# Kernel optimization log

Measured on AMD Instinct MI355X. Metric: run time of the kernel, lower is better.

Reference implementation:

```python
import jax, jax.numpy as jnp
import numpy as np

DIM = 1024
NUM_HEADS = 16
HEAD_DIM = DIM // NUM_HEADS
SCALE = HEAD_DIM ** -0.5


def setup_inputs() -> dict:
    key = jax.random.key(0)
    ks = jax.random.split(key, 5)
    x = jax.random.normal(ks[0], (4, 1024, DIM), dtype=jnp.float32)
    w_qkv = jax.random.normal(ks[1], (DIM, 3 * DIM), dtype=jnp.float32) * (DIM ** -0.5)
    b_qkv = jnp.zeros((3 * DIM,), dtype=jnp.float32)
    w_proj = jax.random.normal(ks[2], (DIM, DIM), dtype=jnp.float32) * (DIM ** -0.5)
    b_proj = jnp.zeros((DIM,), dtype=jnp.float32)
    return {"x": x, "w_qkv": w_qkv, "b_qkv": b_qkv, "w_proj": w_proj, "b_proj": b_proj}


def reference(x, w_qkv, b_qkv, w_proj, b_proj):
    B, N, C = x.shape
    qkv = x @ w_qkv + b_qkv                                  # [B, N, 3C]
    qkv = qkv.reshape(B, N, 3, NUM_HEADS, HEAD_DIM)
    qkv = jnp.transpose(qkv, (2, 0, 3, 1, 4))                # [3, B, H, N, d]
    q, k, v = qkv[0] * SCALE, qkv[1], qkv[2]
    # attn scores in float32 (clamp to finfo range is a no-op after the cast)
    attn = jnp.einsum('bhnd,bhmd->bhnm', q, k).astype(jnp.float32)
    f32 = jnp.finfo(jnp.float32)
    attn = jnp.clip(attn, f32.min, f32.max)
    attn = jax.nn.softmax(attn, axis=-1)
    out = jnp.einsum('bhnm,bhmd->bhnd', attn, v)             # [B, H, N, d]
    out = jnp.transpose(out, (0, 2, 1, 3)).reshape(B, N, C)
    return out @ w_proj + b_proj
```

## Files before the change

kernel.cpp:

```cpp
#include <hip/hip_runtime.h>


typedef _Float16 half8 __attribute__((ext_vector_type(8)));
typedef _Float16 half4v __attribute__((ext_vector_type(4)));
typedef __fp16 fp16x2 __attribute__((ext_vector_type(2)));
typedef float floatx4 __attribute__((ext_vector_type(4)));

#define MFMA16(a, b, c) __builtin_amdgcn_mfma_f32_16x16x32_f16((a), (b), (c), 0, 0, 0)

static constexpr int DIM = 1024;
static constexpr int BATCH = 4;
static constexpr int SEQ = 1024;
static constexpr int NH = 16;
static constexpr int HD = 64;
static constexpr float SCALE = 0.125f;

__device__ static inline void gld16(_Float16* lds, const _Float16* g) {
    __builtin_amdgcn_global_load_lds(
        (const __attribute__((address_space(1))) void*)g,
        (__attribute__((address_space(3))) void*)lds, 16, 0, 0);
}

__global__ __launch_bounds__(256) void prep(const float* __restrict__ x,
                                            _Float16* __restrict__ xh,
                                            const float* __restrict__ wqkv,
                                            _Float16* __restrict__ wqkvT,
                                            const float* __restrict__ wproj,
                                            _Float16* __restrict__ wprojT) {
    __shared__ float tile[32][33];
    const int bid = blockIdx.x;
    const int tid = threadIdx.x;
    if (bid < 4096) {
        int i = (bid * 256 + tid) * 4;
        float4 v = *reinterpret_cast<const float4*>(x + i);
        half4v h;
        h[0] = (_Float16)v.x; h[1] = (_Float16)v.y;
        h[2] = (_Float16)v.z; h[3] = (_Float16)v.w;
        const int m = i >> 10, k = i & 1023;
        *reinterpret_cast<half4v*>(
            &xh[((size_t)(k >> 5) * 4096 + m) * 32 + (k & 31)]) = h;
        return;
    }
    const float* in;
    _Float16* out;
    int C, NN, bx, by;
    if (bid < 7168) {
        int b = bid - 4096;
        in = wqkv; out = wqkvT; C = 3072; NN = 3072;
        bx = b % 96; by = b / 96;
    } else {
        int b = bid - 7168;
        in = wproj; out = wprojT; C = 1024; NN = 1024;
        bx = b & 31; by = b >> 5;
    }
    const int c0 = bx * 32, r0 = by * 32;
    const int tx = tid & 31, ty = tid >> 5;
#pragma unroll
    for (int j = 0; j < 32; j += 8)
        tile[ty + j][tx] = in[(size_t)(r0 + ty + j) * C + (c0 + tx)];
    __syncthreads();
#pragma unroll
    for (int j = 0; j < 32; j += 8)
        out[((size_t)(r0 >> 5) * NN + (c0 + ty + j)) * 32 + tx] =
            (_Float16)tile[tx][ty + j];
}

__global__ __launch_bounds__(512, 2) void gemm_qkv(const _Float16* __restrict__ A,
                                                   const _Float16* __restrict__ Bt,
                                                   const float* __restrict__ bias,
                                                   _Float16* __restrict__ qbuf,
                                                   _Float16* __restrict__ kbuf,
                                                   _Float16* __restrict__ vtbuf) {
    __shared__ __align__(16) _Float16 S[4][14336];

    const int tid = threadIdx.x;
    const int wid = tid >> 6;
    const int lane = tid & 63;
    const int g = lane >> 4;
    const int ln = lane & 15;
    const int wr = wid >> 1, wc = wid & 1;
    const int m0 = blockIdx.y * 256;
    const int n0 = blockIdx.x * 192;
    const bool wlt4 = wid < 4;
    const size_t PA = (size_t)4096 * 32;
    const size_t PB = (size_t)3072 * 32;
    const int lsw = (lane >> 2) * 32 + (((lane & 3) ^ ((lane >> 3) & 3)) * 8);
    const int gsw = (g ^ ((ln >> 1) & 3)) * 8;
    const _Float16* ga0 = A + (size_t)(m0 + wid * 16) * 32 + lsw;
    const _Float16* ga1 = A + (size_t)(m0 + (wid + 8) * 16) * 32 + lsw;
    const _Float16* gb0 = Bt + (size_t)(n0 + wid * 16) * 32 + lsw;
    const _Float16* gb1 = Bt + (size_t)(n0 + (wid + 8) * 16) * 32 + lsw;

    floatx4 acc[4][6];
#pragma unroll
    for (int i = 0; i < 4; ++i)
#pragma unroll
        for (int j = 0; j < 6; ++j) acc[i][j] = (floatx4){0.f, 0.f, 0.f, 0.f};

#define STAGE_A(t)                                                      \
    do {                                                                \
        gld16(&S[(t) & 3][wid * 512], ga0 + (size_t)(t) * PA);          \
        gld16(&S[(t) & 3][(wid + 8) * 512], ga1 + (size_t)(t) * PA);    \
    } while (0)
#define STAGE_B(t)                                                      \
    do {                                                                \
        gld16(&S[(t) & 3][8192 + wid * 512], gb0 + (size_t)(t) * PB);   \
        if (wlt4)                                                       \
            gld16(&S[(t) & 3][8192 + (wid + 8) * 512],                  \
                  gb1 + (size_t)(t) * PB);                              \
    } while (0)

    STAGE_A(0); STAGE_B(0);
    STAGE_A(1); STAGE_B(1);
    STAGE_A(2); STAGE_B(2);

#define COMPUTE_HALF(Sc, hh)                                                   \
    do {                                                                       \
        half8 af[2];                                                           \
        _Pragma("unroll") for (int i = 0; i < 2; ++i) af[i] =                  \
            *reinterpret_cast<const half8*>(                                   \
                &(Sc)[(wr * 64 + (hh) * 32 + i * 16 + ln) * 32 + gsw]);        \
        __builtin_amdgcn_s_setprio(1);                                         \
        _Pragma("unroll") for (int i = 0; i < 2; ++i)                          \
            _Pragma("unroll") for (int j = 0; j < 6; ++j)                      \
                acc[(hh) * 2 + i][j] = MFMA16(af[i], bf[j], acc[(hh) * 2 + i][j]); \
        __builtin_amdgcn_s_setprio(0);                                         \
    } while (0)

#define QKV_STEP(t, DO_STAGE, G4, G3)                                          \
    do {                                                                       \
        if (wlt4) asm volatile("s_waitcnt vmcnt(" G4 ")" ::: "memory");        \
        else      asm volatile("s_waitcnt vmcnt(" G3 ")" ::: "memory");        \
        __builtin_amdgcn_s_barrier();                                          \
        const _Float16* Sc = &S[(t) & 3][0];                                   \
        if (DO_STAGE) STAGE_A((t) + 3);                                        \
        half8 bf[6];                                                           \
        _Pragma("unroll") for (int j = 0; j < 6; ++j) bf[j] =                  \
            *reinterpret_cast<const half8*>(                                   \
                &Sc[8192 + (wc * 96 + j * 16 + ln) * 32 + gsw]);               \
        COMPUTE_HALF(Sc, 0);                                                   \
        if (DO_STAGE) STAGE_B((t) + 3);                                        \
        COMPUTE_HALF(Sc, 1);                                                   \
    } while (0)

    for (int t = 0; t < 29; ++t) QKV_STEP(t, true, "8", "6");
    QKV_STEP(29, false, "8", "6");
    QKV_STEP(30, false, "4", "3");
    QKV_STEP(31, false, "0", "0");

#undef QKV_STEP
#undef COMPUTE_HALF
#undef STAGE_A
#undef STAGE_B

#pragma unroll
    for (int i = 0; i < 4; ++i) {
#pragma unroll
        for (int j = 0; j < 6; ++j) {
            const int n = n0 + wc * 96 + j * 16 + ln;
            const float bn = bias[n];
            const int mrow = m0 + wr * 64 + i * 16 + g * 4;
            const int which = n >> 10;
            const int rem = n & 1023;
            const int h = rem >> 6;
            const int dd = rem & 63;
            const int b = mrow >> 10, tok = mrow & 1023;
            const int bh = b * NH + h;
            if (which == 2) {
                half4v pk;
#pragma unroll
                for (int r = 0; r < 4; ++r) pk[r] = (_Float16)(acc[i][j][r] + bn);
                *reinterpret_cast<half4v*>(
                    &vtbuf[((size_t)(bh * 32 + (tok >> 5)) * 64 + dd) * 32 +
                           (tok & 31)]) = pk;
            } else if (which == 1) {
#pragma unroll
                for (int r = 0; r < 4; ++r)
                    kbuf[((size_t)(bh * 2 + (dd >> 5)) * SEQ + tok + r) * 32 +
                         (dd & 31)] = (_Float16)(acc[i][j][r] + bn);
            } else {
#pragma unroll
                for (int r = 0; r < 4; ++r)
                    qbuf[(size_t)((bh << 10) + tok + r) * HD + dd] =
                        (_Float16)((acc[i][j][r] + bn) * SCALE);
            }
        }
    }
}

__global__ __launch_bounds__(512, 2) void gemm_proj(const _Float16* __restrict__ A,
                                                    const _Float16* __restrict__ Bt,
                                                    const float* __restrict__ bias,
                                                    float* __restrict__ outF) {
    __shared__ __align__(16) _Float16 S[4][8192];

    const int tid = threadIdx.x;
    const int wid = tid >> 6;
    const int lane = tid & 63;
    const int g = lane >> 4;
    const int ln = lane & 15;
    const int wr = wid >> 1, wc = wid & 1;
    const int m0 = blockIdx.y * 128;
    const int n0 = blockIdx.x * 128;
    const size_t PA = (size_t)4096 * 32;
    const size_t PB = (size_t)1024 * 32;
    const int lsw = (lane >> 2) * 32 + (((lane & 3) ^ ((lane >> 3) & 3)) * 8);
    const int gsw = (g ^ ((ln >> 1) & 3)) * 8;
    const _Float16* ga = A + (size_t)(m0 + wid * 16) * 32 + lsw;
    const _Float16* gb = Bt + (size_t)(n0 + wid * 16) * 32 + lsw;

    floatx4 acc[2][4];
#pragma unroll
    for (int i = 0; i < 2; ++i)
#pragma unroll
        for (int j = 0; j < 4; ++j) acc[i][j] = (floatx4){0.f, 0.f, 0.f, 0.f};

#define STAGE_A(t) gld16(&S[(t) & 3][wid * 512], ga + (size_t)(t) * PA)
#define STAGE_B(t) gld16(&S[(t) & 3][4096 + wid * 512], gb + (size_t)(t) * PB)

    STAGE_A(0); STAGE_B(0);
    STAGE_A(1); STAGE_B(1);
    STAGE_A(2); STAGE_B(2);

#define COMPUTE_HALF(Sc, hh)                                                   \
    do {                                                                       \
        half8 af = *reinterpret_cast<const half8*>(                            \
            &(Sc)[(wr * 32 + (hh) * 16 + ln) * 32 + gsw]);                     \
        __builtin_amdgcn_s_setprio(1);                                         \
        _Pragma("unroll") for (int j = 0; j < 4; ++j)                          \
            acc[hh][j] = MFMA16(af, bf[j], acc[hh][j]);                        \
        __builtin_amdgcn_s_setprio(0);                                         \
    } while (0)

#define PROJ_STEP(t, DO_STAGE, GN)                                             \
    do {                                                                       \
        asm volatile("s_waitcnt vmcnt(" GN ")" ::: "memory");                  \
        __builtin_amdgcn_s_barrier();                                          \
        const _Float16* Sc = &S[(t) & 3][0];                                   \
        if (DO_STAGE) STAGE_A((t) + 3);                                        \
        half8 bf[4];                                                           \
        _Pragma("unroll") for (int j = 0; j < 4; ++j) bf[j] =                  \
            *reinterpret_cast<const half8*>(                                   \
                &Sc[4096 + (wc * 64 + j * 16 + ln) * 32 + gsw]);               \
        COMPUTE_HALF(Sc, 0);                                                   \
        if (DO_STAGE) STAGE_B((t) + 3);                                        \
        COMPUTE_HALF(Sc, 1);                                                   \
    } while (0)

    for (int t = 0; t < 29; ++t) PROJ_STEP(t, true, "4");
    PROJ_STEP(29, false, "4");
    PROJ_STEP(30, false, "2");
    PROJ_STEP(31, false, "0");

#undef PROJ_STEP
#undef COMPUTE_HALF
#undef STAGE_A
#undef STAGE_B

#pragma unroll
    for (int i = 0; i < 2; ++i) {
#pragma unroll
        for (int j = 0; j < 4; ++j) {
            const int n = n0 + wc * 64 + j * 16 + ln;
            const float bn = bias[n];
            const int mrow = m0 + wr * 32 + i * 16 + g * 4;
#pragma unroll
            for (int r = 0; r < 4; ++r)
                outF[(size_t)(mrow + r) * 1024 + n] = acc[i][j][r] + bn;
        }
    }
}

__global__ __launch_bounds__(256, 4) void flash_attn(const _Float16* __restrict__ qbuf,
                                                     const _Float16* __restrict__ kbuf,
                                                     const _Float16* __restrict__ vtbuf,
                                                     _Float16* __restrict__ attn_out) {
    __shared__ _Float16 Klds[2 * 4096];
    __shared__ _Float16 Vlds[2 * 4096];

    const int tid = threadIdx.x;
    const int wid = tid >> 6;
    const int lane = tid & 63;
    const int g = lane >> 4;
    const int ln = lane & 15;
    const int bh = blockIdx.x;
    const int qbase = blockIdx.y * 64 + wid * 16;
    const _Float16* qg = qbuf + ((size_t)bh << 10) * HD;
    const _Float16* kg = kbuf + (size_t)bh * (2 * SEQ * 32);
    const _Float16* vg = vtbuf + (size_t)bh * (32 * 64 * 32);

    const int woff = wid * 512;
    const int lsw = (lane >> 2) * 32 + (((lane & 3) ^ ((lane >> 3) & 3)) * 8);
    const int gsw = (g ^ ((ln >> 1) & 3)) * 8;
    const int sl0 = ((lane >> 4) & 1) * 32 + ln;
    const bool hi32 = (lane & 32) != 0;

    half8 qf[2];
#pragma unroll
    for (int f = 0; f < 2; ++f)
        qf[f] = *reinterpret_cast<const half8*>(
            qg + (size_t)(qbase + ln) * HD + f * 32 + g * 8);

    floatx4 o[4];
#pragma unroll
    for (int t = 0; t < 4; ++t) o[t] = (floatx4){0.f, 0.f, 0.f, 0.f};
    float l_lane = 0.f;

    constexpr int NT = SEQ / 64;
#pragma unroll
    for (int f = 0; f < 2; ++f) {
        gld16(&Klds[f * 2048 + woff], kg + (size_t)f * (SEQ * 32) + woff + lsw);
        gld16(&Vlds[f * 2048 + woff], vg + (size_t)f * 2048 + woff + lsw);
    }

    for (int kt = 0; kt < NT; ++kt) {
        asm volatile("s_waitcnt vmcnt(0)" ::: "memory");
        asm volatile("s_barrier" ::: "memory");
        const int cur = kt & 1;
        if (kt < NT - 1) {
            const int nb = cur ^ 1;
#pragma unroll
            for (int f = 0; f < 2; ++f) {
                gld16(&Klds[nb * 4096 + f * 2048 + woff],
                      kg + (size_t)f * (SEQ * 32) + (kt + 1) * 2048 + woff + lsw);
                gld16(&Vlds[nb * 4096 + f * 2048 + woff],
                      vg + (size_t)(2 * (kt + 1) + f) * 2048 + woff + lsw);
            }
        }
        const _Float16* Kb = &Klds[cur * 4096];
        const _Float16* Vb = &Vlds[cur * 4096];

        half8 kf[4][2], vf[4][2];
#pragma unroll
        for (int c = 0; c < 4; ++c)
#pragma unroll
            for (int f = 0; f < 2; ++f) {
                kf[c][f] = *reinterpret_cast<const half8*>(
                    &Kb[f * 2048 + (c * 16 + ln) * 32 + gsw]);
                vf[c][f] = *reinterpret_cast<const half8*>(
                    &Vb[f * 2048 + (c * 16 + ln) * 32 + gsw]);
            }

        floatx4 st[4];
#pragma unroll
        for (int c = 0; c < 4; ++c) {
            floatx4 z = (floatx4){0.f, 0.f, 0.f, 0.f};
            z = MFMA16(kf[c][0], qf[0], z);
            z = MFMA16(kf[c][1], qf[1], z);
            st[c] = z;
        }

        int pk[4][2];
#pragma unroll
        for (int c = 0; c < 4; ++c) {
            float p0 = __expf(st[c][0]);
            float p1 = __expf(st[c][1]);
            float p2 = __expf(st[c][2]);
            float p3 = __expf(st[c][3]);
            l_lane += (p0 + p1) + (p2 + p3);
            union { fp16x2 h; int i; } u0, u1;
            u0.h = __builtin_amdgcn_cvt_pkrtz(p0, p1);
            u1.h = __builtin_amdgcn_cvt_pkrtz(p2, p3);
            pk[c][0] = u0.i;
            pk[c][1] = u1.i;
        }

#pragma unroll
        for (int H = 0; H < 2; ++H) {
            int a0 = __shfl(pk[2 * H][0], sl0), b0 = __shfl(pk[2 * H + 1][0], sl0);
            int a1 = __shfl(pk[2 * H][1], sl0), b1 = __shfl(pk[2 * H + 1][1], sl0);
            int a2 = __shfl(pk[2 * H][0], sl0 + 16), b2 = __shfl(pk[2 * H + 1][0], sl0 + 16);
            int a3 = __shfl(pk[2 * H][1], sl0 + 16), b3 = __shfl(pk[2 * H + 1][1], sl0 + 16);
            union { int i[4]; half8 h; } ua;
            ua.i[0] = hi32 ? b0 : a0;
            ua.i[1] = hi32 ? b1 : a1;
            ua.i[2] = hi32 ? b2 : a2;
            ua.i[3] = hi32 ? b3 : a3;
#pragma unroll
            for (int t = 0; t < 4; ++t) o[t] = MFMA16(ua.h, vf[t][H], o[t]);
        }
    }

    l_lane += __shfl_xor(l_lane, 16);
    l_lane += __shfl_xor(l_lane, 32);

    const int b = bh >> 4, h = bh & 15;
#pragma unroll
    for (int r = 0; r < 4; ++r) {
        const float inv = 1.0f / __shfl(l_lane, g * 4 + r);
        const int tok = qbase + g * 4 + r;
#pragma unroll
        for (int t = 0; t < 4; ++t)
            attn_out[((size_t)(h * 2 + (t >> 1)) * 4096 + (b * SEQ + tok)) * 32 +
                     (t & 1) * 16 + ln] = (_Float16)(o[t][r] * inv);
    }
}

extern "C" void kernel_launch(void* const* d_in, const int* in_sizes, int n_in,
                              void* d_out, int out_size, void* d_ws, size_t ws_size,
                              hipStream_t stream) {
    const float* x = (const float*)d_in[0];
    const float* wqkv = (const float*)d_in[1];
    const float* bqkv = (const float*)d_in[2];
    const float* wproj = (const float*)d_in[3];
    const float* bproj = (const float*)d_in[4];
    float* out = (float*)d_out;

    char* ws = (char*)d_ws;
    _Float16* xh     = (_Float16*)(ws);
    _Float16* wqkvT  = (_Float16*)(ws + (8ull << 20));
    _Float16* qbuf   = (_Float16*)(ws + (14ull << 20));
    _Float16* kbuf   = (_Float16*)(ws + (22ull << 20));
    _Float16* vtbuf  = (_Float16*)(ws + (30ull << 20));
    _Float16* wprojT = (_Float16*)(ws + (38ull << 20));
    _Float16* attn   = xh;

    prep<<<8192, 256, 0, stream>>>(x, xh, wqkv, wqkvT, wproj, wprojT);
    gemm_qkv<<<dim3(16, 16), 512, 0, stream>>>(xh, wqkvT, bqkv, qbuf, kbuf, vtbuf);
    flash_attn<<<dim3(BATCH * NH, SEQ / 64), 256, 0, stream>>>(qbuf, kbuf, vtbuf, attn);
    gemm_proj<<<dim3(8, 32), 512, 0, stream>>>(attn, wprojT, bproj, out);
}
```

Baseline: 163.1 us.

## Process two query tiles per wave in flash attention to reuse K/V fragments

```diff
diff --git a/kernel.cpp b/kernel.cpp
--- a/kernel.cpp
+++ b/kernel.cpp
@@ -271,7 +271,7 @@
     }
 }
 
-__global__ __launch_bounds__(256, 4) void flash_attn(const _Float16* __restrict__ qbuf,
+__global__ __launch_bounds__(256, 2) void flash_attn(const _Float16* __restrict__ qbuf,
                                                      const _Float16* __restrict__ kbuf,
                                                      const _Float16* __restrict__ vtbuf,
                                                      _Float16* __restrict__ attn_out) {
@@ -284,7 +284,7 @@
     const int g = lane >> 4;
     const int ln = lane & 15;
     const int bh = blockIdx.x;
-    const int qbase = blockIdx.y * 64 + wid * 16;
+    const int qbase = blockIdx.y * 128 + wid * 32;
     const _Float16* qg = qbuf + ((size_t)bh << 10) * HD;
     const _Float16* kg = kbuf + (size_t)bh * (2 * SEQ * 32);
     const _Float16* vg = vtbuf + (size_t)bh * (32 * 64 * 32);
@@ -295,16 +295,22 @@
     const int sl0 = ((lane >> 4) & 1) * 32 + ln;
     const bool hi32 = (lane & 32) != 0;
 
-    half8 qf[2];
-#pragma unroll
-    for (int f = 0; f < 2; ++f)
-        qf[f] = *reinterpret_cast<const half8*>(
+    half8 qfA[2], qfB[2];
+#pragma unroll
+    for (int f = 0; f < 2; ++f) {
+        qfA[f] = *reinterpret_cast<const half8*>(
             qg + (size_t)(qbase + ln) * HD + f * 32 + g * 8);
-
-    floatx4 o[4];
-#pragma unroll
-    for (int t = 0; t < 4; ++t) o[t] = (floatx4){0.f, 0.f, 0.f, 0.f};
-    float l_lane = 0.f;
+        qfB[f] = *reinterpret_cast<const half8*>(
+            qg + (size_t)(qbase + 16 + ln) * HD + f * 32 + g * 8);
+    }
+
+    floatx4 oA[4], oB[4];
+#pragma unroll
+    for (int t = 0; t < 4; ++t) {
+        oA[t] = (floatx4){0.f, 0.f, 0.f, 0.f};
+        oB[t] = (floatx4){0.f, 0.f, 0.f, 0.f};
+    }
+    float lA = 0.f, lB = 0.f;
 
     constexpr int NT = SEQ / 64;
 #pragma unroll
@@ -341,58 +347,90 @@
                     &Vb[f * 2048 + (c * 16 + ln) * 32 + gsw]);
             }
 
-        floatx4 st[4];
+        int pkA[4][2], pkB[4][2];
 #pragma unroll
         for (int c = 0; c < 4; ++c) {
             floatx4 z = (floatx4){0.f, 0.f, 0.f, 0.f};
-            z = MFMA16(kf[c][0], qf[0], z);
-            z = MFMA16(kf[c][1], qf[1], z);
-            st[c] = z;
-        }
-
-        int pk[4][2];
-#pragma unroll
-        for (int c = 0; c < 4; ++c) {
-            float p0 = __expf(st[c][0]);
-            float p1 = __expf(st[c][1]);
-            float p2 = __expf(st[c][2]);
-            float p3 = __expf(st[c][3]);
-            l_lane += (p0 + p1) + (p2 + p3);
+            z = MFMA16(kf[c][0], qfA[0], z);
+            z = MFMA16(kf[c][1], qfA[1], z);
+            float p0 = __expf(z[0]);
+            float p1 = __expf(z[1]);
+            float p2 = __expf(z[2]);
+            float p3 = __expf(z[3]);
+            lA += (p0 + p1) + (p2 + p3);
             union { fp16x2 h; int i; } u0, u1;
             u0.h = __builtin_amdgcn_cvt_pkrtz(p0, p1);
             u1.h = __builtin_amdgcn_cvt_pkrtz(p2, p3);
-            pk[c][0] = u0.i;
-            pk[c][1] = u1.i;
+            pkA[c][0] = u0.i;
+            pkA[c][1] = u1.i;
+        }
+#pragma unroll
+        for (int c = 0; c < 4; ++c) {
+            floatx4 z = (floatx4){0.f, 0.f, 0.f, 0.f};
+            z = MFMA16(kf[c][0], qfB[0], z);
+            z = MFMA16(kf[c][1], qfB[1], z);
+            float p0 = __expf(z[0]);
+            float p1 = __expf(z[1]);
+            float p2 = __expf(z[2]);
+            float p3 = __expf(z[3]);
+            lB += (p0 + p1) + (p2 + p3);
+            union { fp16x2 h; int i; } u0, u1;
+            u0.h = __builtin_amdgcn_cvt_pkrtz(p0, p1);
+            u1.h = __builtin_amdgcn_cvt_pkrtz(p2, p3);
+            pkB[c][0] = u0.i;
+            pkB[c][1] = u1.i;
         }
 
 #pragma unroll
         for (int H = 0; H < 2; ++H) {
-            int a0 = __shfl(pk[2 * H][0], sl0), b0 = __shfl(pk[2 * H + 1][0], sl0);
-            int a1 = __shfl(pk[2 * H][1], sl0), b1 = __shfl(pk[2 * H + 1][1], sl0);
-            int a2 = __shfl(pk[2 * H][0], sl0 + 16), b2 = __shfl(pk[2 * H + 1][0], sl0 + 16);
-            int a3 = __shfl(pk[2 * H][1], sl0 + 16), b3 = __shfl(pk[2 * H + 1][1], sl0 + 16);
-            union { int i[4]; half8 h; } ua;
-            ua.i[0] = hi32 ? b0 : a0;
-            ua.i[1] = hi32 ? b1 : a1;
-            ua.i[2] = hi32 ? b2 : a2;
-            ua.i[3] = hi32 ? b3 : a3;
-#pragma unroll
-            for (int t = 0; t < 4; ++t) o[t] = MFMA16(ua.h, vf[t][H], o[t]);
-        }
-    }
-
-    l_lane += __shfl_xor(l_lane, 16);
-    l_lane += __shfl_xor(l_lane, 32);
+            {
+                int a0 = __shfl(pkA[2 * H][0], sl0), b0 = __shfl(pkA[2 * H + 1][0], sl0);
+                int a1 = __shfl(pkA[2 * H][1], sl0), b1 = __shfl(pkA[2 * H + 1][1], sl0);
+                int a2 = __shfl(pkA[2 * H][0], sl0 + 16), b2 = __shfl(pkA[2 * H + 1][0], sl0 + 16);
+                int a3 = __shfl(pkA[2 * H][1], sl0 + 16), b3 = __shfl(pkA[2 * H + 1][1], sl0 + 16);
+                union { int i[4]; half8 h; } ua;
+                ua.i[0] = hi32 ? b0 : a0;
+                ua.i[1] = hi32 ? b1 : a1;
+                ua.i[2] = hi32 ? b2 : a2;
+                ua.i[3] = hi32 ? b3 : a3;
+#pragma unroll
+                for (int t = 0; t < 4; ++t) oA[t] = MFMA16(ua.h, vf[t][H], oA[t]);
+            }
+            {
+                int a0 = __shfl(pkB[2 * H][0], sl0), b0 = __shfl(pkB[2 * H + 1][0], sl0);
+                int a1 = __shfl(pkB[2 * H][1], sl0), b1 = __shfl(pkB[2 * H + 1][1], sl0);
+                int a2 = __shfl(pkB[2 * H][0], sl0 + 16), b2 = __shfl(pkB[2 * H + 1][0], sl0 + 16);
+                int a3 = __shfl(pkB[2 * H][1], sl0 + 16), b3 = __shfl(pkB[2 * H + 1][1], sl0 + 16);
+                union { int i[4]; half8 h; } ua;
+                ua.i[0] = hi32 ? b0 : a0;
+                ua.i[1] = hi32 ? b1 : a1;
+                ua.i[2] = hi32 ? b2 : a2;
+                ua.i[3] = hi32 ? b3 : a3;
+#pragma unroll
+                for (int t = 0; t < 4; ++t) oB[t] = MFMA16(ua.h, vf[t][H], oB[t]);
+            }
+        }
+    }
+
+    lA += __shfl_xor(lA, 16);
+    lA += __shfl_xor(lA, 32);
+    lB += __shfl_xor(lB, 16);
+    lB += __shfl_xor(lB, 32);
 
     const int b = bh >> 4, h = bh & 15;
 #pragma unroll
     for (int r = 0; r < 4; ++r) {
-        const float inv = 1.0f / __shfl(l_lane, g * 4 + r);
-        const int tok = qbase + g * 4 + r;
-#pragma unroll
-        for (int t = 0; t < 4; ++t)
-            attn_out[((size_t)(h * 2 + (t >> 1)) * 4096 + (b * SEQ + tok)) * 32 +
-                     (t & 1) * 16 + ln] = (_Float16)(o[t][r] * inv);
+        const float invA = 1.0f / __shfl(lA, g * 4 + r);
+        const float invB = 1.0f / __shfl(lB, g * 4 + r);
+        const int tokA = qbase + g * 4 + r;
+        const int tokB = tokA + 16;
+#pragma unroll
+        for (int t = 0; t < 4; ++t) {
+            attn_out[((size_t)(h * 2 + (t >> 1)) * 4096 + (b * SEQ + tokA)) * 32 +
+                     (t & 1) * 16 + ln] = (_Float16)(oA[t][r] * invA);
+            attn_out[((size_t)(h * 2 + (t >> 1)) * 4096 + (b * SEQ + tokB)) * 32 +
+                     (t & 1) * 16 + ln] = (_Float16)(oB[t][r] * invB);
+        }
     }
 }
 
@@ -417,6 +455,6 @@
 
     prep<<<8192, 256, 0, stream>>>(x, xh, wqkv, wqkvT, wproj, wprojT);
     gemm_qkv<<<dim3(16, 16), 512, 0, stream>>>(xh, wqkvT, bqkv, qbuf, kbuf, vtbuf);
-    flash_attn<<<dim3(BATCH * NH, SEQ / 64), 256, 0, stream>>>(qbuf, kbuf, vtbuf, attn);
+    flash_attn<<<dim3(BATCH * NH, SEQ / 128), 256, 0, stream>>>(qbuf, kbuf, vtbuf, attn);
     gemm_proj<<<dim3(8, 32), 512, 0, stream>>>(attn, wprojT, bproj, out);
 }
```

Measured after the change: 162.6 us (median of 2 runs). Within noise of the previous version (-0.4%).
